# Kernel tuning notes

Hardware: AMD Instinct MI355X
Metric: run time of the kernel (lower is better)

## Reference

```python
import jax, jax.numpy as jnp
import numpy as np

B, T, V = 8, 1024, 10000
BLANK = 0  # original code treats token id 0 as the CTC blank


def setup_inputs() -> dict:
    key = jax.random.key(0)
    k1, k2 = jax.random.split(key)
    logits = jax.random.normal(k1, (B, T, V), dtype=jnp.float32)
    lengths = jax.random.randint(k2, (B,), 0, T, dtype=jnp.int32)
    return {"logits": logits, "lengths": lengths}


def reference(logits, lengths):
    """CTC greedy decode: log_softmax + argmax, then vectorized blank/duplicate collapse.

    Equivalent to the original per-sample Python loop: a frame t (with t < length)
    is kept iff preds[t] != BLANK and preds[t] != preds[t-1]. (The original's
    `blank` flag -- keep a repeat if a blank intervened -- is subsumed because an
    intervening blank makes preds[t-1] == BLANK != preds[t].)

    Returns (tokens, out_len, scores):
      tokens  [B, T] int32 -- collapsed token ids, left-packed, zero-padded
      out_len [B]    int32 -- number of emitted tokens per sample
      scores  [B]    float32 -- sum of max log-probs over kept frames (greedy path score)
    """
    logp = jax.nn.log_softmax(logits, axis=-1)          # [B, T, V]
    preds = jnp.argmax(logp, axis=-1).astype(jnp.int32)  # [B, T]
    maxlogp = jnp.max(logp, axis=-1)                      # [B, T]

    t_idx = jnp.arange(T, dtype=jnp.int32)[None, :]       # [1, T]
    valid = t_idx < lengths[:, None]                      # [B, T]
    prev = jnp.pad(preds[:, :-1], ((0, 0), (1, 0)), constant_values=BLANK)
    keep = valid & (preds != BLANK) & (preds != prev)     # [B, T]

    # left-pack kept tokens via cumsum positions + scatter (dropped frames -> col T)
    pos = jnp.cumsum(keep.astype(jnp.int32), axis=1) - 1  # [B, T]
    scatter_pos = jnp.where(keep, pos, T)
    b_idx = jnp.arange(B, dtype=jnp.int32)[:, None]
    tokens = jnp.zeros((B, T + 1), dtype=jnp.int32)
    tokens = tokens.at[b_idx, scatter_pos].set(jnp.where(keep, preds, 0))
    tokens = tokens[:, :T]

    out_len = jnp.sum(keep, axis=1).astype(jnp.int32)
    scores = jnp.sum(jnp.where(keep, maxlogp, 0.0), axis=1)
    return tokens, out_len, scores
```

## Files before the change

kernel.cpp:

```cpp
#include <hip/hip_runtime.h>
#include <math.h>

#define B_ 8
#define T_ 1024
#define V_ 10000
#define NV4 (V_ / 4)
#define BLANK_ 0

__global__ __launch_bounds__(256) void frame_reduce_kernel(
    const float* __restrict__ logits,
    int*   __restrict__ preds,
    float* __restrict__ mlp,
    float* __restrict__ tokens)
{
    const int frame = blockIdx.x;
    const int tid   = threadIdx.x;
    const float4* row = (const float4*)(logits + (size_t)frame * V_);

    float m = -INFINITY;
    float s = 0.0f;
    int   idx = 0;

    for (int i = tid; i < NV4; i += 256) {
        float4 v4 = row[i];
        float vv[4] = {v4.x, v4.y, v4.z, v4.w};
#pragma unroll
        for (int c = 0; c < 4; ++c) {
            float v = vv[c];
            float d = v - m;
            float e = __expf(-fabsf(d));
            if (d > 0.0f) {
                s = s * e + 1.0f;
                m = v;
                idx = i * 4 + c;
            } else {
                s += e;
            }
        }
    }

#pragma unroll
    for (int off = 32; off > 0; off >>= 1) {
        float m2 = __shfl_down(m, off);
        float s2 = __shfl_down(s, off);
        int   i2 = __shfl_down(idx, off);
        if (m2 > m || (m2 == m && i2 < idx)) {
            s = s2 + s * __expf(m - m2);
            m = m2;
            idx = i2;
        } else {
            s = s + s2 * __expf(m2 - m);
        }
    }

    __shared__ float sm[4], ss[4];
    __shared__ int   si[4];
    const int wave = tid >> 6;
    if ((tid & 63) == 0) { sm[wave] = m; ss[wave] = s; si[wave] = idx; }
    __syncthreads();
    if (tid == 0) {
#pragma unroll
        for (int w = 1; w < 4; ++w) {
            float m2 = sm[w], s2 = ss[w];
            int   i2 = si[w];
            if (m2 > m || (m2 == m && i2 < idx)) {
                s = s2 + s * __expf(m - m2);
                m = m2;
                idx = i2;
            } else {
                s = s + s2 * __expf(m2 - m);
            }
        }
        preds[frame]  = idx;
        mlp[frame]    = -__logf(s);
        tokens[frame] = 0.0f;
    }
}

__global__ __launch_bounds__(64) void collapse_kernel(
    const int*   __restrict__ preds,
    const float* __restrict__ mlp,
    const int*   __restrict__ lengths,
    float* __restrict__ tokens,
    float* __restrict__ out_len,
    float* __restrict__ scores)
{
    const int b    = blockIdx.x;
    const int lane = threadIdx.x;
    const int len  = lengths[b];
    const int* prow = preds + b * T_;
    const float* srow = mlp + b * T_;
    float* trow = tokens + b * T_;

    int   base = 0;
    float score_acc = 0.0f;

#pragma unroll 1
    for (int chunk = 0; chunk < T_ / 64; ++chunk) {
        const int t = chunk * 64 + lane;
        const int p    = prow[t];
        const int prev = (t == 0) ? BLANK_ : prow[t - 1];
        const bool keep = (t < len) && (p != BLANK_) && (p != prev);
        const unsigned long long mask = __ballot(keep);
        const int pos = base + __popcll(mask & ((1ull << lane) - 1ull));
        if (keep) {
            trow[pos] = (float)p;
            score_acc += srow[t];
        }
        base += __popcll(mask);
    }

#pragma unroll
    for (int off = 32; off > 0; off >>= 1)
        score_acc += __shfl_down(score_acc, off);

    if (lane == 0) {
        out_len[b] = (float)base;
        scores[b]  = score_acc;
    }
}

extern "C" void kernel_launch(void* const* d_in, const int* in_sizes, int n_in,
                              void* d_out, int out_size, void* d_ws, size_t ws_size,
                              hipStream_t stream) {
    const float* logits  = (const float*)d_in[0];
    const int*   lengths = (const int*)d_in[1];

    float* out_f  = (float*)d_out;
    float* tokens = out_f;
    float* outlen = out_f + B_ * T_;
    float* scores = out_f + B_ * T_ + B_;

    int*   preds = (int*)d_ws;
    float* mlp   = (float*)((char*)d_ws + (size_t)B_ * T_ * sizeof(int));

    frame_reduce_kernel<<<B_ * T_, 256, 0, stream>>>(logits, preds, mlp, tokens);
    collapse_kernel<<<B_, 64, 0, stream>>>(preds, mlp, lengths, tokens, outlen, scores);
}
```

Baseline: 437.3 us.

## Register-cache frame row, two-pass max then exp2 sum, unrolled collapse

Each thread now loads its full slice of the frame row (10 float4) into registers with nontemporal loads up front. The online softmax with a branch per element is replaced by a two-pass scheme: a max/argmax pass over four independent lanes, then an exp2-based sum. The collapse kernel preloads all preds and scores into registers and gets the previous token through a lane shuffle instead of a second global load. This removes the dependent serial exp chain and exposes memory-level parallelism, at the cost of higher register use per thread.

```diff
diff --git a/kernel.cpp b/kernel.cpp
--- a/kernel.cpp
+++ b/kernel.cpp
@@ -4,8 +4,23 @@
 #define B_ 8
 #define T_ 1024
 #define V_ 10000
-#define NV4 (V_ / 4)
+#define NV4 2500
 #define BLANK_ 0
+#define LOG2E 1.44269504088896340736f
+#define LN2   0.69314718055994530942f
+
+typedef float vf4 __attribute__((ext_vector_type(4)));
+
+#if __has_builtin(__builtin_amdgcn_exp2f)
+#define EXP2F(x) __builtin_amdgcn_exp2f(x)
+#else
+#define EXP2F(x) exp2f(x)
+#endif
+#if __has_builtin(__builtin_amdgcn_logf)
+#define LOG2F(x) __builtin_amdgcn_logf(x)
+#else
+#define LOG2F(x) log2f(x)
+#endif
 
 __global__ __launch_bounds__(256) void frame_reduce_kernel(
     const float* __restrict__ logits,
@@ -15,41 +30,53 @@
 {
     const int frame = blockIdx.x;
     const int tid   = threadIdx.x;
-    const float4* row = (const float4*)(logits + (size_t)frame * V_);
+    const vf4* row = (const vf4*)(logits + (size_t)frame * V_);
 
-    float m = -INFINITY;
-    float s = 0.0f;
-    int   idx = 0;
+    vf4 r[10];
+#pragma unroll
+    for (int k = 0; k < 9; ++k)
+        r[k] = __builtin_nontemporal_load(&row[tid + k * 256]);
+    r[9] = (vf4){-INFINITY, -INFINITY, -INFINITY, -INFINITY};
+    if (tid + 2304 < NV4)
+        r[9] = __builtin_nontemporal_load(&row[tid + 2304]);
 
-    for (int i = tid; i < NV4; i += 256) {
-        float4 v4 = row[i];
-        float vv[4] = {v4.x, v4.y, v4.z, v4.w};
+    float m0 = -INFINITY, m1 = -INFINITY, m2 = -INFINITY, m3 = -INFINITY;
+    int   i0 = 0x7fffffff, i1 = 0x7fffffff, i2 = 0x7fffffff, i3 = 0x7fffffff;
 #pragma unroll
-        for (int c = 0; c < 4; ++c) {
-            float v = vv[c];
-            float d = v - m;
-            float e = __expf(-fabsf(d));
-            if (d > 0.0f) {
-                s = s * e + 1.0f;
-                m = v;
-                idx = i * 4 + c;
-            } else {
-                s += e;
-            }
-        }
+    for (int k = 0; k < 10; ++k) {
+        const int gi = (tid + k * 256) * 4;
+        if (r[k].x > m0) { m0 = r[k].x; i0 = gi + 0; }
+        if (r[k].y > m1) { m1 = r[k].y; i1 = gi + 1; }
+        if (r[k].z > m2) { m2 = r[k].z; i2 = gi + 2; }
+        if (r[k].w > m3) { m3 = r[k].w; i3 = gi + 3; }
     }
+    float m = m0;
+    int   idx = i0;
+    if (m1 > m || (m1 == m && i1 < idx)) { m = m1; idx = i1; }
+    if (m2 > m || (m2 == m && i2 < idx)) { m = m2; idx = i2; }
+    if (m3 > m || (m3 == m && i3 < idx)) { m = m3; idx = i3; }
+
+    const float mK = m * LOG2E;
+    float s0 = 0.0f, s1 = 0.0f, s2 = 0.0f, s3 = 0.0f;
+#pragma unroll
+    for (int k = 0; k < 10; ++k) {
+        s0 += EXP2F(__builtin_fmaf(r[k].x, LOG2E, -mK));
+        s1 += EXP2F(__builtin_fmaf(r[k].y, LOG2E, -mK));
+        s2 += EXP2F(__builtin_fmaf(r[k].z, LOG2E, -mK));
+        s3 += EXP2F(__builtin_fmaf(r[k].w, LOG2E, -mK));
+    }
+    float s = (s0 + s1) + (s2 + s3);
 
 #pragma unroll
     for (int off = 32; off > 0; off >>= 1) {
-        float m2 = __shfl_down(m, off);
-        float s2 = __shfl_down(s, off);
-        int   i2 = __shfl_down(idx, off);
-        if (m2 > m || (m2 == m && i2 < idx)) {
-            s = s2 + s * __expf(m - m2);
-            m = m2;
-            idx = i2;
+        float mo = __shfl_down(m, off);
+        float so = __shfl_down(s, off);
+        int   io = __shfl_down(idx, off);
+        if (mo > m || (mo == m && io < idx)) {
+            s = so + s * EXP2F((m - mo) * LOG2E);
+            m = mo; idx = io;
         } else {
-            s = s + s2 * __expf(m2 - m);
+            s = s + so * EXP2F((mo - m) * LOG2E);
         }
     }
 
@@ -61,18 +88,17 @@
     if (tid == 0) {
 #pragma unroll
         for (int w = 1; w < 4; ++w) {
-            float m2 = sm[w], s2 = ss[w];
-            int   i2 = si[w];
-            if (m2 > m || (m2 == m && i2 < idx)) {
-                s = s2 + s * __expf(m - m2);
-                m = m2;
-                idx = i2;
+            float mo = sm[w], so = ss[w];
+            int   io = si[w];
+            if (mo > m || (mo == m && io < idx)) {
+                s = so + s * EXP2F((m - mo) * LOG2E);
+                m = mo; idx = io;
             } else {
-                s = s + s2 * __expf(m2 - m);
+                s = s + so * EXP2F((mo - m) * LOG2E);
             }
         }
         preds[frame]  = idx;
-        mlp[frame]    = -__logf(s);
+        mlp[frame]    = -LOG2F(s) * LN2;
         tokens[frame] = 0.0f;
     }
 }
@@ -88,35 +114,45 @@
     const int b    = blockIdx.x;
     const int lane = threadIdx.x;
     const int len  = lengths[b];
-    const int* prow = preds + b * T_;
-    const float* srow = mlp + b * T_;
+    const int*   prow = preds + b * T_;
+    const float* srow = mlp   + b * T_;
     float* trow = tokens + b * T_;
 
-    int   base = 0;
-    float score_acc = 0.0f;
+    int   p_r[16];
+    float s_r[16];
+#pragma unroll
+    for (int c = 0; c < 16; ++c) {
+        p_r[c] = prow[c * 64 + lane];
+        s_r[c] = srow[c * 64 + lane];
+    }
 
-#pragma unroll 1
-    for (int chunk = 0; chunk < T_ / 64; ++chunk) {
-        const int t = chunk * 64 + lane;
-        const int p    = prow[t];
-        const int prev = (t == 0) ? BLANK_ : prow[t - 1];
+    int   base  = 0;
+    int   carry = BLANK_;
+    float acc   = 0.0f;
+#pragma unroll
+    for (int c = 0; c < 16; ++c) {
+        const int t = c * 64 + lane;
+        const int p = p_r[c];
+        int prev = __shfl_up(p, 1);
+        if (lane == 0) prev = carry;
+        carry = __shfl(p, 63);
         const bool keep = (t < len) && (p != BLANK_) && (p != prev);
         const unsigned long long mask = __ballot(keep);
         const int pos = base + __popcll(mask & ((1ull << lane) - 1ull));
         if (keep) {
             trow[pos] = (float)p;
-            score_acc += srow[t];
+            acc += s_r[c];
         }
         base += __popcll(mask);
     }
 
 #pragma unroll
     for (int off = 32; off > 0; off >>= 1)
-        score_acc += __shfl_down(score_acc, off);
+        acc += __shfl_down(acc, off);
 
     if (lane == 0) {
         out_len[b] = (float)base;
-        scores[b]  = score_acc;
+        scores[b]  = acc;
     }
 }
 
@@ -132,8 +168,8 @@
     float* scores = out_f + B_ * T_ + B_;
 
     int*   preds = (int*)d_ws;
-    float* mlp   = (float*)((char*)d_ws + (size_t)B_ * T_ * sizeof(int));
+    float* mlpws = (float*)((char*)d_ws + (size_t)B_ * T_ * sizeof(int));
 
-    frame_reduce_kernel<<<B_ * T_, 256, 0, stream>>>(logits, preds, mlp, tokens);
-    collapse_kernel<<<B_, 64, 0, stream>>>(preds, mlp, lengths, tokens, outlen, scores);
+    frame_reduce_kernel<<<B_ * T_, 256, 0, stream>>>(logits, preds, mlpws, tokens);
+    collapse_kernel<<<B_, 64, 0, stream>>>(preds, mlpws, lengths, tokens, outlen, scores);
 }
```

After: 403.3 us. -7.8%, faster.
